# Kernel optimization log

Measured on AMD Instinct MI355X. Metric: run time of the kernel, lower is better.

Reference implementation:

```python
import jax, jax.numpy as jnp
import numpy as np

H = 16       # num_heads (groups for complex conv)
A = 32       # num frequency anchors
KSZ = 5      # complex conv kernel size
PAD = (KSZ - 1) // 2  # circular padding, matches ComplexConv1DLayer


def setup_inputs() -> dict:
    key = jax.random.key(0)
    ks = jax.random.split(key, 12)
    B, N, D = 4, 2048, 1024
    hid, ghid = 256, 256  # pooling MLP hidden, gate MLP hidden
    F = N // 2 + 1

    def rn(k, shp, s=0.02):
        return jax.random.normal(k, shp, jnp.float32) * s

    return {
        "x": jax.random.normal(ks[0], (B, N, D), jnp.float32),
        "Wv": rn(ks[1], (D, D)), "bv": jnp.zeros((D,), jnp.float32),
        "Wp1": rn(ks[2], (D, hid)), "bp1": jnp.zeros((hid,), jnp.float32),
        "Wp2": rn(ks[3], (hid, 1)), "bp2": jnp.zeros((1,), jnp.float32),
        "Wg1": rn(ks[4], (D, ghid)), "bg1": jnp.zeros((ghid,), jnp.float32),
        "Wg2": rn(ks[5], (ghid, 2 * H * A)), "bg2": jnp.zeros((2 * H * A,), jnp.float32),
        "mod_bias": jnp.zeros((F,), jnp.float32),
        "conv_kr": rn(ks[6], (KSZ,), 1.0 / np.sqrt(KSZ)),
        "conv_ki": rn(ks[7], (KSZ,), 1.0 / np.sqrt(KSZ)),
        "Wo": rn(ks[8], (D, D)), "bo": jnp.zeros((D,), jnp.float32),
    }


def reference(x, Wv, bv, Wp1, bp1, Wp2, bp2, Wg1, bg1, Wg2, bg2,
              mod_bias, conv_kr, conv_ki, Wo, bo):
    B, N, D = x.shape
    dh = D // H
    F = N // 2 + 1

    # value projection -> per-head sequences, rFFT over sequence axis
    v = (x @ Wv + bv).reshape(B, N, H, dh).transpose(0, 2, 1, 3)   # (B,H,N,dh)
    Vf = jnp.fft.rfft(v, axis=2)                                   # (B,H,F,dh) complex64

    # AttentionPoolingLayer: two-layer MLP scores -> softmax over seq -> weighted sum
    s = jax.nn.gelu(x @ Wp1 + bp1, approximate=False) @ Wp2 + bp2  # (B,N,1)
    w = jax.nn.softmax(s, axis=1)
    g = jnp.sum(x * w, axis=1)                                     # (B,D)

    # gate MLP -> complex anchors (B,H,A)
    a = (jax.nn.gelu(g @ Wg1 + bg1, approximate=False) @ Wg2 + bg2).reshape(B, H, A, 2)
    anch_r, anch_i = a[..., 0], a[..., 1]

    # ComplexInterpolationLayer: cubic interpolation of anchors to F bins
    gr = jax.image.resize(anch_r, (B, H, F), method="cubic")
    gi = jax.image.resize(anch_i, (B, H, F), method="cubic")
    gate = gr + 1j * gi                                            # (B,H,F)

    # ComplexModReLULayer: ReLU(|z|+b) * z / |z| with per-frequency bias
    mag = jnp.abs(gate)
    gate = gate * (jax.nn.relu(mag + mod_bias) / (mag + 1e-8))

    # ComplexConv1DLayer: circular-pad complex conv along frequency
    gp = jnp.concatenate([gate[..., -PAD:], gate, gate[..., :PAD]], axis=-1)
    ker = conv_kr.astype(jnp.complex64) + 1j * conv_ki.astype(jnp.complex64)
    gate = sum(ker[j] * gp[..., j:j + F] for j in range(KSZ))      # (B,H,F)

    # spectral gating + inverse FFT + output projection
    y = jnp.fft.irfft(Vf * gate[..., None], n=N, axis=2)           # (B,H,N,dh)
    y = y.transpose(0, 2, 1, 3).reshape(B, N, D)
    return y @ Wo + bo
```

## Files before the change

kernel.cpp:

```cpp
#include <hip/hip_runtime.h>
#include <math.h>

#define NSEQ 2048
#define DMOD 1024
#define NBATCH 4
#define NHEAD 16
#define NFREQ 1025

typedef unsigned short u16t;
typedef __attribute__((ext_vector_type(8))) short short8;
typedef __attribute__((ext_vector_type(4))) float f32x4;

__device__ __forceinline__ float gelu_exact(float x) {
  return 0.5f * x * (1.0f + erff(x * 0.70710678118654752440f));
}
__device__ __forceinline__ u16t bf16_rtn(float x) {
  unsigned u = __float_as_uint(x);
  return (u16t)((u + 0x7FFFu + ((u >> 16) & 1u)) >> 16);
}
__device__ __forceinline__ float bf16f(u16t h) {
  return __uint_as_float(((unsigned)h) << 16);
}
__device__ __forceinline__ void gload_lds16(const u16t* g, u16t* l) {
  __builtin_amdgcn_global_load_lds(
      (const __attribute__((address_space(1))) void*)g,
      (__attribute__((address_space(3))) void*)l, 16, 0, 0);
}

__global__ __launch_bounds__(256) void split_kernel(const float* __restrict__ in,
    u16t* __restrict__ hi, u16t* __restrict__ lo, int n8) {
  for (int i = blockIdx.x * blockDim.x + threadIdx.x; i < n8; i += gridDim.x * blockDim.x) {
    const float4* p = reinterpret_cast<const float4*>(in + (size_t)i * 8);
    float4 a = p[0], b = p[1];
    float vv[8] = {a.x, a.y, a.z, a.w, b.x, b.y, b.z, b.w};
    alignas(16) u16t th[8];
    alignas(16) u16t tl[8];
#pragma unroll
    for (int e = 0; e < 8; ++e) {
      u16t h = bf16_rtn(vv[e]);
      th[e] = h;
      tl[e] = bf16_rtn(vv[e] - bf16f(h));
    }
    *reinterpret_cast<uint4*>(hi + (size_t)i * 8) = *reinterpret_cast<const uint4*>(th);
    *reinterpret_cast<uint4*>(lo + (size_t)i * 8) = *reinterpret_cast<const uint4*>(tl);
  }
}

__global__ __launch_bounds__(256) void tsplit_kernel(const float* __restrict__ W,
    u16t* __restrict__ Th, u16t* __restrict__ Tl, int K, int N) {
  __shared__ float tile[32][33];
  int k0 = blockIdx.y * 32, n0 = blockIdx.x * 32;
  int r = threadIdx.x >> 5, c = threadIdx.x & 31;
#pragma unroll
  for (int i = 0; i < 4; ++i)
    tile[r + 8 * i][c] = W[(size_t)(k0 + r + 8 * i) * N + n0 + c];
  __syncthreads();
#pragma unroll
  for (int i = 0; i < 4; ++i) {
    int rr = r + 8 * i;
    float v = tile[c][rr];
    u16t h = bf16_rtn(v);
    Th[(size_t)(n0 + rr) * K + k0 + c] = h;
    Tl[(size_t)(n0 + rr) * K + k0 + c] = bf16_rtn(v - bf16f(h));
  }
}

__global__ __launch_bounds__(256) void gemm_fused_kernel(
    const u16t* __restrict__ Ah_g, const u16t* __restrict__ Al_g,
    const u16t* __restrict__ Bvh, const u16t* __restrict__ Bvl,
    const u16t* __restrict__ Bph, const u16t* __restrict__ Bpl,
    const float* __restrict__ bv, const float* __restrict__ bp1,
    const float* __restrict__ Wp2,
    float* __restrict__ vT, float* __restrict__ s_part) {
  __shared__ u16t Ahs[128 * 64], Als[128 * 64], Bhs[128 * 64], Bls[128 * 64];
  __shared__ u16t Php[32 * 64], Ppl[32 * 64];
  const int tid = threadIdx.x;
  const int lane = tid & 63, wave = tid >> 6;
  const int lr = lane & 15, lg = lane >> 4;
  const int wm0 = (wave >> 1) * 64, wn0 = (wave & 1) * 64;
  const int nwg = gridDim.x;
  const int L = (blockIdx.x & 7) * (nwg >> 3) + (blockIdx.x >> 3);
  const int m0 = (L >> 3) * 128;
  const int nblk = L & 7;
  const int n0 = nblk * 128;
  const int pc0 = nblk * 32;
  const int K = 1024;

  f32x4 acc[4][4];
#pragma unroll
  for (int i = 0; i < 4; ++i)
#pragma unroll
    for (int j = 0; j < 4; ++j) acc[i][j] = 0.0f;
  f32x4 accp[2][2];
#pragma unroll
  for (int i = 0; i < 2; ++i)
#pragma unroll
    for (int j = 0; j < 2; ++j) accp[i][j] = 0.0f;

  for (int k0 = 0; k0 < K; k0 += 64) {
#pragma unroll
    for (int q = 0; q < 4; ++q) {
      int cid = q * 256 + tid;
      int row = cid >> 3, grp = cid & 7;
      int koff = k0 + ((grp ^ (row & 7)) << 3);
      size_t ea = (size_t)(m0 + row) * K + koff;
      size_t eb = (size_t)(n0 + row) * K + koff;
      int lbase = q * 2048 + wave * 512;
      gload_lds16(Ah_g + ea, Ahs + lbase);
      gload_lds16(Al_g + ea, Als + lbase);
      gload_lds16(Bvh + eb, Bhs + lbase);
      gload_lds16(Bvl + eb, Bls + lbase);
    }
    {
      int row = tid >> 3, grp = tid & 7;
      int koff = k0 + ((grp ^ (row & 7)) << 3);
      size_t ep = (size_t)(pc0 + row) * K + koff;
      int lbase = wave * 512;
      gload_lds16(Bph + ep, Php + lbase);
      gload_lds16(Bpl + ep, Ppl + lbase);
    }
    __syncthreads();
#pragma unroll
    for (int kf = 0; kf < 2; ++kf) {
      short8 ah[4], al[4];
#pragma unroll
      for (int mi = 0; mi < 4; ++mi) {
        int r_ = wm0 + mi * 16 + lr;
        int g = (kf * 4 + lg) ^ (r_ & 7);
        ah[mi] = *reinterpret_cast<const short8*>(&Ahs[r_ * 64 + g * 8]);
        al[mi] = *reinterpret_cast<const short8*>(&Als[r_ * 64 + g * 8]);
      }
#pragma unroll
      for (int ni = 0; ni < 4; ++ni) {
        int r_ = wn0 + ni * 16 + lr;
        int g = (kf * 4 + lg) ^ (r_ & 7);
        short8 bh8 = *reinterpret_cast<const short8*>(&Bhs[r_ * 64 + g * 8]);
        short8 bl8 = *reinterpret_cast<const short8*>(&Bls[r_ * 64 + g * 8]);
#pragma unroll
        for (int mi = 0; mi < 4; ++mi) {
          acc[mi][ni] = __builtin_amdgcn_mfma_f32_16x16x32_bf16(ah[mi], bh8, acc[mi][ni], 0, 0, 0);
          acc[mi][ni] = __builtin_amdgcn_mfma_f32_16x16x32_bf16(ah[mi], bl8, acc[mi][ni], 0, 0, 0);
          acc[mi][ni] = __builtin_amdgcn_mfma_f32_16x16x32_bf16(al[mi], bh8, acc[mi][ni], 0, 0, 0);
        }
      }
      short8 pah[2], pal[2];
#pragma unroll
      for (int mi = 0; mi < 2; ++mi) {
        int r_ = wave * 32 + mi * 16 + lr;
        int g = (kf * 4 + lg) ^ (r_ & 7);
        pah[mi] = *reinterpret_cast<const short8*>(&Ahs[r_ * 64 + g * 8]);
        pal[mi] = *reinterpret_cast<const short8*>(&Als[r_ * 64 + g * 8]);
      }
#pragma unroll
      for (int ni = 0; ni < 2; ++ni) {
        int r_ = ni * 16 + lr;
        int g = (kf * 4 + lg) ^ (r_ & 7);
        short8 pbh = *reinterpret_cast<const short8*>(&Php[r_ * 64 + g * 8]);
        short8 pbl = *reinterpret_cast<const short8*>(&Ppl[r_ * 64 + g * 8]);
#pragma unroll
        for (int mi = 0; mi < 2; ++mi) {
          accp[mi][ni] = __builtin_amdgcn_mfma_f32_16x16x32_bf16(pah[mi], pbh, accp[mi][ni], 0, 0, 0);
          accp[mi][ni] = __builtin_amdgcn_mfma_f32_16x16x32_bf16(pah[mi], pbl, accp[mi][ni], 0, 0, 0);
          accp[mi][ni] = __builtin_amdgcn_mfma_f32_16x16x32_bf16(pal[mi], pbh, accp[mi][ni], 0, 0, 0);
        }
      }
    }
    __syncthreads();
  }
#pragma unroll
  for (int mi = 0; mi < 4; ++mi)
#pragma unroll
    for (int ni = 0; ni < 4; ++ni) {
      int col = n0 + wn0 + ni * 16 + lr;
      float bvv = bv[col];
      f32x4 a = acc[mi][ni];
      int mbase = m0 + wm0 + mi * 16 + lg * 4;
      int b = mbase >> 11, ss = mbase & 2047;
      float4 o4;
      o4.x = a[0] + bvv; o4.y = a[1] + bvv; o4.z = a[2] + bvv; o4.w = a[3] + bvv;
      *reinterpret_cast<float4*>(vT + (size_t)b * (DMOD * NSEQ) + (size_t)col * NSEQ + ss) = o4;
    }
  {
    float w2[2], bcol[2];
#pragma unroll
    for (int ni = 0; ni < 2; ++ni) {
      int col = pc0 + ni * 16 + lr;
      w2[ni] = Wp2[col];
      bcol[ni] = bp1[col];
    }
#pragma unroll
    for (int mi = 0; mi < 2; ++mi)
#pragma unroll
      for (int r = 0; r < 4; ++r) {
        float p = 0.f;
#pragma unroll
        for (int ni = 0; ni < 2; ++ni)
          p = fmaf(gelu_exact(accp[mi][ni][r] + bcol[ni]), w2[ni], p);
        p += __shfl_xor(p, 1);
        p += __shfl_xor(p, 2);
        p += __shfl_xor(p, 4);
        p += __shfl_xor(p, 8);
        if (lr == 0) {
          int row = m0 + wave * 32 + mi * 16 + lg * 4 + r;
          s_part[nblk * 8192 + row] = p;
        }
      }
  }
}

template<int NBLK>
__global__ __launch_bounds__(256) void mfma_gemm(
    const u16t* __restrict__ Ah_g, const u16t* __restrict__ Al_g,
    const u16t* __restrict__ Bh_g, const u16t* __restrict__ Bl_g,
    const float* __restrict__ bias,
    float* __restrict__ Cf,
    int N, int K) {
  __shared__ u16t Ahs[128 * 64], Als[128 * 64], Bhs[128 * 64], Bls[128 * 64];
  const int tid = threadIdx.x;
  const int lane = tid & 63, wave = tid >> 6;
  const int lr = lane & 15, lg = lane >> 4;
  const int wm0 = (wave >> 1) * 64, wn0 = (wave & 1) * 64;
  const int nwg = gridDim.x;
  const int L = (blockIdx.x & 7) * (nwg >> 3) + (blockIdx.x >> 3);
  const int m0 = (L / NBLK) * 128, n0 = (L % NBLK) * 128;

  f32x4 acc[4][4];
#pragma unroll
  for (int i = 0; i < 4; ++i)
#pragma unroll
    for (int j = 0; j < 4; ++j) acc[i][j] = 0.0f;

  for (int k0 = 0; k0 < K; k0 += 64) {
#pragma unroll
    for (int q = 0; q < 4; ++q) {
      int cid = q * 256 + tid;
      int row = cid >> 3, grp = cid & 7;
      int koff = k0 + ((grp ^ (row & 7)) << 3);
      size_t ea = (size_t)(m0 + row) * K + koff;
      size_t eb = (size_t)(n0 + row) * K + koff;
      int lbase = q * 2048 + wave * 512;
      gload_lds16(Ah_g + ea, Ahs + lbase);
      gload_lds16(Al_g + ea, Als + lbase);
      gload_lds16(Bh_g + eb, Bhs + lbase);
      gload_lds16(Bl_g + eb, Bls + lbase);
    }
    __syncthreads();
#pragma unroll
    for (int kf = 0; kf < 2; ++kf) {
      short8 ah[4], al[4];
#pragma unroll
      for (int mi = 0; mi < 4; ++mi) {
        int r_ = wm0 + mi * 16 + lr;
        int g = (kf * 4 + lg) ^ (r_ & 7);
        ah[mi] = *reinterpret_cast<const short8*>(&Ahs[r_ * 64 + g * 8]);
        al[mi] = *reinterpret_cast<const short8*>(&Als[r_ * 64 + g * 8]);
      }
#pragma unroll
      for (int ni = 0; ni < 4; ++ni) {
        int r_ = wn0 + ni * 16 + lr;
        int g = (kf * 4 + lg) ^ (r_ & 7);
        short8 bh8 = *reinterpret_cast<const short8*>(&Bhs[r_ * 64 + g * 8]);
        short8 bl8 = *reinterpret_cast<const short8*>(&Bls[r_ * 64 + g * 8]);
#pragma unroll
        for (int mi = 0; mi < 4; ++mi) {
          acc[mi][ni] = __builtin_amdgcn_mfma_f32_16x16x32_bf16(ah[mi], bh8, acc[mi][ni], 0, 0, 0);
          acc[mi][ni] = __builtin_amdgcn_mfma_f32_16x16x32_bf16(ah[mi], bl8, acc[mi][ni], 0, 0, 0);
          acc[mi][ni] = __builtin_amdgcn_mfma_f32_16x16x32_bf16(al[mi], bh8, acc[mi][ni], 0, 0, 0);
        }
      }
    }
    __syncthreads();
  }
#pragma unroll
  for (int mi = 0; mi < 4; ++mi)
#pragma unroll
    for (int ni = 0; ni < 4; ++ni) {
      int col = n0 + wn0 + ni * 16 + lr;
      float bvv = bias[col];
      f32x4 a = acc[mi][ni];
#pragma unroll
      for (int r = 0; r < 4; ++r) {
        int row = m0 + wm0 + mi * 16 + lg * 4 + r;
        Cf[(size_t)row * N + col] = a[r] + bvv;
      }
    }
}

#define PADI(i) ((i) + ((i) >> 5))

template<int HJ, int TWS>
__device__ __forceinline__ void fwd_reg_stage(float* vr, float* vi,
    const float* TWr, const float* TWi, int lane) {
  float twr_[HJ], twi_[HJ];
#pragma unroll
  for (int t = 0; t < HJ; ++t) {
    int m = (t * 64 + lane) * TWS;
    twr_[t] = TWr[PADI(m)]; twi_[t] = TWi[PADI(m)];
  }
#pragma unroll
  for (int j = 0; j < 16; ++j) {
    if (j & HJ) continue;
    int t = j & (HJ - 1);
    float ur = vr[j], ui = vi[j];
    float wr = vr[j + HJ], wi = vi[j + HJ];
    float dr = ur - wr, di = ui - wi;
    vr[j] = ur + wr; vi[j] = ui + wi;
    vr[j + HJ] = dr * twr_[t] - di * twi_[t];
    vi[j + HJ] = dr * twi_[t] + di * twr_[t];
  }
}

template<int S, int TWS>
__device__ __forceinline__ void fwd_lane_stage(float* vr, float* vi,
    const float* TWr, const float* TWi, int lane) {
  float twr_ = 1.0f, twi_ = 0.0f;
  if (S > 1) {
    int m = (lane & (S - 1)) * TWS;
    twr_ = TWr[PADI(m)]; twi_ = TWi[PADI(m)];
  }
  bool hi = (lane & S) != 0;
#pragma unroll
  for (int j = 0; j < 16; ++j) {
    float or_ = __shfl_xor(vr[j], S, 64);
    float oi_ = __shfl_xor(vi[j], S, 64);
    float sr = vr[j] + or_, si_ = vi[j] + oi_;
    float dr = or_ - vr[j], di = oi_ - vi[j];
    float rr = dr * twr_ - di * twi_;
    float ri = dr * twi_ + di * twr_;
    vr[j] = hi ? rr : sr;
    vi[j] = hi ? ri : si_;
  }
}

template<int S, int TWS>
__device__ __forceinline__ void inv_lane_stage(float* vr, float* vi,
    const float* TWr, const float* TWi, int lane) {
  float twr_ = 1.0f, twi_ = 0.0f;
  if (S > 1) {
    int m = (lane & (S - 1)) * TWS;
    twr_ = TWr[PADI(m)]; twi_ = -TWi[PADI(m)];
  }
  bool hi = (lane & S) != 0;
#pragma unroll
  for (int j = 0; j < 16; ++j) {
    float xr = vr[j], xi = vi[j];
    if (S > 1) {
      float pr = xr * twr_ - xi * twi_;
      float pi = xr * twi_ + xi * twr_;
      xr = hi ? pr : xr;
      xi = hi ? pi : xi;
    }
    float or_ = __shfl_xor(xr, S, 64);
    float oi_ = __shfl_xor(xi, S, 64);
    vr[j] = hi ? (or_ - xr) : (xr + or_);
    vi[j] = hi ? (oi_ - xi) : (xi + oi_);
  }
}

template<int HJ, int TWS>
__device__ __forceinline__ void inv_reg_stage(float* vr, float* vi,
    const float* TWr, const float* TWi, int lane) {
  float twr_[HJ], twi_[HJ];
#pragma unroll
  for (int t = 0; t < HJ; ++t) {
    int m = (t * 64 + lane) * TWS;
    twr_[t] = TWr[PADI(m)]; twi_[t] = -TWi[PADI(m)];
  }
#pragma unroll
  for (int j = 0; j < 16; ++j) {
    if (j & HJ) continue;
    int t = j & (HJ - 1);
    float ur = vr[j], ui = vi[j];
    float br = vr[j + HJ], bi = vi[j + HJ];
    float wr = br * twr_[t] - bi * twi_[t];
    float wi = br * twi_[t] + bi * twr_[t];
    vr[j] = ur + wr; vi[j] = ui + wi;
    vr[j + HJ] = ur - wr; vi[j + HJ] = ui - wi;
  }
}

__global__ __launch_bounds__(256) void conv_fft_kernel(
    float* __restrict__ vio, const float* __restrict__ gateb) {
  __shared__ float Zr[4][1056], Zi[4][1056];
  __shared__ float TWr[528], TWi[528];
  const int tid = threadIdx.x;
  const int lane = tid & 63, wave = tid >> 6;
  const int c0 = blockIdx.x * 4;
  const int b = blockIdx.y;
  const int bh = b * NHEAD + (c0 >> 6);
  const float* gate_bh = gateb + (size_t)bh * NFREQ * 2;

#pragma unroll
  for (int q = 0; q < 2; ++q) {
    int m = q * 256 + tid;
    float si, co;
    sincosf(-3.14159265358979323846f * (float)m * (1.0f / 512.0f), &si, &co);
    TWr[PADI(m)] = co; TWi[PADI(m)] = si;
  }
  __syncthreads();

  float* zr = Zr[wave];
  float* zi = Zi[wave];
  float* col = vio + ((size_t)b * DMOD + (c0 + wave)) * NSEQ;

  float vr[16], vi[16];
#pragma unroll
  for (int j = 0; j < 16; ++j) {
    float2 w2 = *reinterpret_cast<const float2*>(col + 2 * (j * 64 + lane));
    vr[j] = w2.x; vi[j] = w2.y;
  }

  fwd_reg_stage<8, 1>(vr, vi, TWr, TWi, lane);
  fwd_reg_stage<4, 2>(vr, vi, TWr, TWi, lane);
  fwd_reg_stage<2, 4>(vr, vi, TWr, TWi, lane);
  fwd_reg_stage<1, 8>(vr, vi, TWr, TWi, lane);
  fwd_lane_stage<32, 16>(vr, vi, TWr, TWi, lane);
  fwd_lane_stage<16, 32>(vr, vi, TWr, TWi, lane);
  fwd_lane_stage<8, 64>(vr, vi, TWr, TWi, lane);
  fwd_lane_stage<4, 128>(vr, vi, TWr, TWi, lane);
  fwd_lane_stage<2, 256>(vr, vi, TWr, TWi, lane);
  fwd_lane_stage<1, 0>(vr, vi, TWr, TWi, lane);

#pragma unroll
  for (int j = 0; j < 16; ++j) {
    int p = PADI(j * 64 + lane);
    zr[p] = vr[j]; zi[p] = vi[j];
  }
  asm volatile("s_waitcnt lgkmcnt(0)" ::: "memory");

  const float s1 = 1.0f / 1024.0f;
#pragma unroll
  for (int q = 0; q < 8; ++q) {
    int k = q * 64 + lane;
    if (k == 0) {
      float z0r = zr[0], z0i = zi[0];
      float X0 = z0r + z0i;
      float XN = z0r - z0i;
      float2 G0 = *reinterpret_cast<const float2*>(gate_bh + 0);
      float2 GN = *reinterpret_cast<const float2*>(gate_bh + 1024 * 2);
      float y0 = X0 * G0.x * s1;
      float yN = XN * GN.x * s1;
      zr[0] = 0.5f * (y0 + yN); zi[0] = 0.5f * (y0 - yN);
      float zmr = zr[1], zmi = zi[1];
      float X5r = zmr, X5i = -zmi;
      float2 G5 = *reinterpret_cast<const float2*>(gate_bh + 512 * 2);
      float Y5r = (X5r * G5.x - X5i * G5.y) * s1;
      float Y5i = (X5r * G5.y + X5i * G5.x) * s1;
      zr[1] = Y5r; zi[1] = -Y5i;
    } else {
      int kq = 1024 - k;
      int rp = PADI((int)(__brev((unsigned)k) >> 22));
      int rq = PADI((int)(__brev((unsigned)kq) >> 22));
      float Zkr = zr[rp], Zki = zi[rp];
      float Zqr = zr[rq], Zqi = zi[rq];
      float Er = 0.5f * (Zkr + Zqr), Ei = 0.5f * (Zki - Zqi);
      float Odr = 0.5f * (Zki + Zqi), Odi = -0.5f * (Zkr - Zqr);
      float ti, tr;
      sincosf(-3.14159265358979323846f * (float)k * (1.0f / 1024.0f), &ti, &tr);
      float Pr = Odr * tr - Odi * ti, Pi = Odr * ti + Odi * tr;
      float Xkr = Er + Pr, Xki = Ei + Pi;
      float Xqr = Er - Pr, Xqi = -(Ei - Pi);
      float2 Gk = *reinterpret_cast<const float2*>(gate_bh + k * 2);
      float2 Gq = *reinterpret_cast<const float2*>(gate_bh + kq * 2);
      float Ykr = (Xkr * Gk.x - Xki * Gk.y) * s1;
      float Yki = (Xkr * Gk.y + Xki * Gk.x) * s1;
      float Yqr = (Xqr * Gq.x - Xqi * Gq.y) * s1;
      float Yqi = (Xqr * Gq.y + Xqi * Gq.x) * s1;
      float E2r = 0.5f * (Ykr + Yqr), E2i = 0.5f * (Yki - Yqi);
      float D2r = 0.5f * (Ykr - Yqr), D2i = 0.5f * (Yki + Yqi);
      float O2r = D2r * tr + D2i * ti, O2i = D2i * tr - D2r * ti;
      zr[rp] = E2r - O2i; zi[rp] = E2i + O2r;
      zr[rq] = E2r + O2i; zi[rq] = O2r - E2i;
    }
  }
  asm volatile("s_waitcnt lgkmcnt(0)" ::: "memory");

#pragma unroll
  for (int j = 0; j < 16; ++j) {
    int p = PADI(j * 64 + lane);
    vr[j] = zr[p]; vi[j] = zi[p];
  }
  asm volatile("s_waitcnt lgkmcnt(0)" ::: "memory");

  inv_lane_stage<1, 0>(vr, vi, TWr, TWi, lane);
  inv_lane_stage<2, 256>(vr, vi, TWr, TWi, lane);
  inv_lane_stage<4, 128>(vr, vi, TWr, TWi, lane);
  inv_lane_stage<8, 64>(vr, vi, TWr, TWi, lane);
  inv_lane_stage<16, 32>(vr, vi, TWr, TWi, lane);
  inv_lane_stage<32, 16>(vr, vi, TWr, TWi, lane);
  inv_reg_stage<1, 8>(vr, vi, TWr, TWi, lane);
  inv_reg_stage<2, 4>(vr, vi, TWr, TWi, lane);
  inv_reg_stage<4, 2>(vr, vi, TWr, TWi, lane);
  inv_reg_stage<8, 1>(vr, vi, TWr, TWi, lane);

#pragma unroll
  for (int j = 0; j < 16; ++j) {
    *reinterpret_cast<float2*>(col + 2 * (j * 64 + lane)) = make_float2(vr[j], vi[j]);
  }
}

__global__ __launch_bounds__(256) void tysplit_kernel(
    const float* __restrict__ yT, u16t* __restrict__ yh, u16t* __restrict__ yl) {
  __shared__ float tile[64][65];
  int t0 = blockIdx.x * 64, c0 = blockIdx.y * 64, b = blockIdx.z;
  int r = threadIdx.x >> 4;
  int cc = (threadIdx.x & 15) * 4;
#pragma unroll
  for (int i = 0; i < 4; ++i) {
    int row = r + 16 * i;
    float4 w = *reinterpret_cast<const float4*>(
        yT + ((size_t)b * DMOD + c0 + row) * NSEQ + t0 + cc);
    tile[row][cc] = w.x; tile[row][cc + 1] = w.y;
    tile[row][cc + 2] = w.z; tile[row][cc + 3] = w.w;
  }
  __syncthreads();
#pragma unroll
  for (int i = 0; i < 4; ++i) {
    int tt = r + 16 * i;
    alignas(8) u16t hh[4], ll[4];
#pragma unroll
    for (int e = 0; e < 4; ++e) {
      float v = tile[cc + e][tt];
      u16t h = bf16_rtn(v);
      hh[e] = h;
      ll[e] = bf16_rtn(v - bf16f(h));
    }
    size_t o = ((size_t)b * NSEQ + t0 + tt) * DMOD + c0 + cc;
    *reinterpret_cast<ushort4*>(yh + o) = *reinterpret_cast<const ushort4*>(hh);
    *reinterpret_cast<ushort4*>(yl + o) = *reinterpret_cast<const ushort4*>(ll);
  }
}

__global__ __launch_bounds__(256) void softmax_stats_kernel(
    const float* __restrict__ s_part, const float* __restrict__ bp2,
    float* __restrict__ s, float* __restrict__ bstats) {
  int b = blockIdx.x, tid = threadIdx.x;
  __shared__ float red[256];
  float bp = bp2[0];
  float m = -1e30f;
  for (int n = tid; n < NSEQ; n += 256) {
    int row = b * NSEQ + n;
    float v = bp;
#pragma unroll
    for (int c = 0; c < 8; ++c) v += s_part[c * 8192 + row];
    s[row] = v;
    m = fmaxf(m, v);
  }
  red[tid] = m; __syncthreads();
  for (int o = 128; o; o >>= 1) { if (tid < o) red[tid] = fmaxf(red[tid], red[tid + o]); __syncthreads(); }
  float bm = red[0]; __syncthreads();
  float sum = 0.f;
  for (int n = tid; n < NSEQ; n += 256) sum += expf(s[b * NSEQ + n] - bm);
  red[tid] = sum; __syncthreads();
  for (int o = 128; o; o >>= 1) { if (tid < o) red[tid] += red[tid + o]; __syncthreads(); }
  if (tid == 0) { bstats[b * 2] = bm; bstats[b * 2 + 1] = red[0]; }
}

__global__ __launch_bounds__(256) void pool_partial_kernel(
    const float* __restrict__ x, const float* __restrict__ s,
    const float* __restrict__ bstats, float* __restrict__ gpart) {
  int chunk = blockIdx.x, b = blockIdx.y;
  int tid = threadIdx.x;
  __shared__ float wsh[128];
  float bm = bstats[b * 2], inv = 1.0f / bstats[b * 2 + 1];
  int n0 = chunk * 128;
  if (tid < 128) wsh[tid] = expf(s[b * NSEQ + n0 + tid] - bm) * inv;
  __syncthreads();
  float acc[4] = {};
  for (int n = 0; n < 128; ++n) {
    float wn = wsh[n];
    const float* xr = &x[((size_t)b * NSEQ + n0 + n) * DMOD];
#pragma unroll
    for (int q = 0; q < 4; ++q) acc[q] = fmaf(wn, xr[tid + 256 * q], acc[q]);
  }
  float* gp = &gpart[((size_t)b * 16 + chunk) * DMOD];
#pragma unroll
  for (int q = 0; q < 4; ++q) gp[tid + 256 * q] = acc[q];
}

__global__ __launch_bounds__(256) void pool_reduce_mlp1_kernel(
    const float* __restrict__ gpart, const float* __restrict__ Wg1,
    float* __restrict__ part1) {
  int kb = blockIdx.x, b = blockIdx.y;
  int tid = threadIdx.x;
  int k0 = kb * 64;
  __shared__ float g_s[64];
  if (tid < 64) {
    float acc = 0.f;
#pragma unroll
    for (int j = 0; j < 16; ++j)
      acc += gpart[((size_t)b * 16 + j) * DMOD + k0 + tid];
    g_s[tid] = acc;
  }
  __syncthreads();
  float acc = 0.f;
#pragma unroll 8
  for (int i = 0; i < 64; ++i)
    acc = fmaf(g_s[i], Wg1[(size_t)(k0 + i) * 256 + tid], acc);
  part1[((size_t)b * 16 + kb) * 256 + tid] = acc;
}

__global__ __launch_bounds__(256) void mlp1red_mlp2_kernel(
    const float* __restrict__ part1, const float* __restrict__ bg1,
    const float* __restrict__ Wg2, float* __restrict__ part2) {
  int kb2 = blockIdx.x, nh = blockIdx.y, b = blockIdx.z;
  int tid = threadIdx.x;
  int k0 = kb2 * 64;
  __shared__ float hs_s[64];
  if (tid < 64) {
    float acc = bg1[k0 + tid];
#pragma unroll
    for (int j = 0; j < 16; ++j)
      acc += part1[((size_t)b * 16 + j) * 256 + k0 + tid];
    hs_s[tid] = gelu_exact(acc);
  }
  __syncthreads();
  float acc[2] = {};
#pragma unroll 8
  for (int i = 0; i < 64; ++i) {
    float hv = hs_s[i];
    const float* wr = &Wg2[(size_t)(k0 + i) * 1024 + nh * 512];
    acc[0] = fmaf(hv, wr[tid], acc[0]);
    acc[1] = fmaf(hv, wr[tid + 256], acc[1]);
  }
  float* pp = &part2[((size_t)b * 4 + kb2) * 1024 + nh * 512];
  pp[tid] = acc[0];
  pp[tid + 256] = acc[1];
}

__device__ __forceinline__ float keys_cubic(float x) {
  if (x >= 2.0f) return 0.0f;
  if (x >= 1.0f) return ((-0.5f * x + 2.5f) * x - 4.0f) * x + 2.0f;
  return ((1.5f * x - 2.5f) * x) * x + 1.0f;
}

__global__ __launch_bounds__(256) void gate_kernel(
    const float* __restrict__ part2, const float* __restrict__ bg2,
    const float* __restrict__ mod_bias,
    const float* __restrict__ kr5, const float* __restrict__ ki5,
    float* __restrict__ gate_out) {
  int bh = blockIdx.x;
  int tid = threadIdx.x;
  __shared__ float anch_s[64];
  __shared__ float ar_[32], ai_[32];
  __shared__ float gr[NFREQ], gi[NFREQ];
  int b = bh >> 4, h = bh & 15;
  if (tid < 64) {
    int cc = h * 64 + tid;
    float acc = bg2[cc];
#pragma unroll
    for (int j = 0; j < 4; ++j)
      acc += part2[((size_t)b * 4 + j) * 1024 + cc];
    anch_s[tid] = acc;
  }
  __syncthreads();
  if (tid < 32) {
    ar_[tid] = anch_s[tid * 2 + 0];
    ai_[tid] = anch_s[tid * 2 + 1];
  }
  __syncthreads();
  const float inv_scale = 32.0f / 1025.0f;
  for (int f = tid; f < NFREQ; f += 256) {
    float c = (f + 0.5f) * inv_scale - 0.5f;
    int j0 = (int)floorf(c) - 1;
    float wr = 0.f, wi = 0.f, wsum = 0.f;
#pragma unroll
    for (int u = 0; u < 4; ++u) {
      int j = j0 + u;
      if (j < 0 || j > 31) continue;
      float w = keys_cubic(fabsf(c - (float)j));
      wsum += w;
      wr = fmaf(w, ar_[j], wr);
      wi = fmaf(w, ai_[j], wi);
    }
    float invw = 1.0f / wsum;
    wr *= invw; wi *= invw;
    float mag = sqrtf(wr * wr + wi * wi);
    float scale = fmaxf(mag + mod_bias[f], 0.0f) / (mag + 1e-8f);
    gr[f] = wr * scale;
    gi[f] = wi * scale;
  }
  __syncthreads();
  float k_r[5], k_i[5];
#pragma unroll
  for (int j = 0; j < 5; ++j) { k_r[j] = kr5[j]; k_i[j] = ki5[j]; }
  for (int f = tid; f < NFREQ; f += 256) {
    float cr = 0.f, ci = 0.f;
#pragma unroll
    for (int j = 0; j < 5; ++j) {
      int idx = f + j - 2;
      if (idx < 0) idx += NFREQ;
      else if (idx >= NFREQ) idx -= NFREQ;
      float a = gr[idx], bb = gi[idx];
      cr = fmaf(k_r[j], a, cr); cr = fmaf(-k_i[j], bb, cr);
      ci = fmaf(k_r[j], bb, ci); ci = fmaf(k_i[j], a, ci);
    }
    gate_out[((size_t)bh * NFREQ + f) * 2 + 0] = cr;
    gate_out[((size_t)bh * NFREQ + f) * 2 + 1] = ci;
  }
}

extern "C" void kernel_launch(void* const* d_in, const int* in_sizes, int n_in,
                              void* d_out, int out_size, void* d_ws, size_t ws_size,
                              hipStream_t stream) {
  const float* x        = (const float*)d_in[0];
  const float* Wv       = (const float*)d_in[1];
  const float* bv       = (const float*)d_in[2];
  const float* Wp1      = (const float*)d_in[3];
  const float* bp1      = (const float*)d_in[4];
  const float* Wp2      = (const float*)d_in[5];
  const float* bp2      = (const float*)d_in[6];
  const float* Wg1      = (const float*)d_in[7];
  const float* bg1      = (const float*)d_in[8];
  const float* Wg2      = (const float*)d_in[9];
  const float* bg2      = (const float*)d_in[10];
  const float* mod_bias = (const float*)d_in[11];
  const float* ckr      = (const float*)d_in[12];
  const float* cki      = (const float*)d_in[13];
  const float* Wo       = (const float*)d_in[14];
  const float* bo       = (const float*)d_in[15];

  const int M = NBATCH * NSEQ;
  const size_t MD = (size_t)M * DMOD;
  char* wsb = (char*)d_ws;

  u16t* x_hi = (u16t*)wsb;
  u16t* x_lo = x_hi + MD;
  u16t* y_hi = x_hi;
  u16t* y_lo = x_lo;
  u16t* WT_h = (u16t*)(wsb + (size_t)32 * 1024 * 1024);
  u16t* WT_l = (u16t*)(wsb + (size_t)34 * 1024 * 1024);
  u16t* WTp1_h = (u16t*)(wsb + (size_t)36 * 1024 * 1024);
  u16t* WTp1_l = (u16t*)(wsb + (size_t)36 * 1024 * 1024 + 524288);
  float* s_part = (float*)(wsb + (size_t)37 * 1024 * 1024);
  float* s      = (float*)(wsb + (size_t)36 * 1024 * 1024);
  float* bstats = s + 8192;
  float* gpart  = bstats + 16;
  float* part1 = (float*)(wsb + (size_t)32 * 1024 * 1024);
  float* part2 = part1 + 4 * 16 * 256;
  float* gateb = (float*)(wsb + (size_t)32 * 1024 * 1024 + 65536);

  float* vT  = (float*)d_out;
  float* out = (float*)d_out;

  dim3 blk(256);

  split_kernel<<<dim3(2048), blk, 0, stream>>>(x, x_hi, x_lo, (int)(MD / 8));
  tsplit_kernel<<<dim3(1024 / 32, 1024 / 32), blk, 0, stream>>>(Wv, WT_h, WT_l, 1024, 1024);
  tsplit_kernel<<<dim3(256 / 32, 1024 / 32), blk, 0, stream>>>(Wp1, WTp1_h, WTp1_l, 1024, 256);
  gemm_fused_kernel<<<dim3(512), blk, 0, stream>>>(
      x_hi, x_lo, WT_h, WT_l, WTp1_h, WTp1_l, bv, bp1, Wp2, vT, s_part);
  softmax_stats_kernel<<<dim3(NBATCH), blk, 0, stream>>>(s_part, bp2, s, bstats);
  pool_partial_kernel<<<dim3(16, NBATCH), blk, 0, stream>>>(x, s, bstats, gpart);
  pool_reduce_mlp1_kernel<<<dim3(16, NBATCH), blk, 0, stream>>>(gpart, Wg1, part1);
  mlp1red_mlp2_kernel<<<dim3(4, 2, NBATCH), blk, 0, stream>>>(part1, bg1, Wg2, part2);
  gate_kernel<<<dim3(NBATCH * NHEAD), blk, 0, stream>>>(part2, bg2, mod_bias, ckr, cki, gateb);
  conv_fft_kernel<<<dim3(DMOD / 4, NBATCH), blk, 0, stream>>>(vT, gateb);
  tysplit_kernel<<<dim3(NSEQ / 64, DMOD / 64, NBATCH), blk, 0, stream>>>(vT, y_hi, y_lo);
  tsplit_kernel<<<dim3(1024 / 32, 1024 / 32), blk, 0, stream>>>(Wo, WT_h, WT_l, 1024, 1024);
  mfma_gemm<8><<<dim3((DMOD / 128) * (M / 128)), blk, 0, stream>>>(
      y_hi, y_lo, WT_h, WT_l, bo, out, DMOD, 1024);
}
```

Before: 206.0 us.

## Fuse small pooling/gate kernels and merge weight-split launches to cut launch count

Merges the Wv and Wp1 transpose-split launches into one kernel and folds the softmax statistics into each pool_partial block, which now recomputes the per-batch max and sum redundantly. It also moves the second gate MLP layer into gate_kernel and drops the separate mlp1red_mlp2 launch. The Wo split is moved earlier, into the slot after the fused GEMM, and workspace pointers are re-laid out so its buffers do not collide. The aim is fewer tiny serialized launches, at the cost of redundant softmax work in every block and a serial 256-term dot product per thread in gate_kernel.

```diff
diff --git a/kernel.cpp b/kernel.cpp
--- a/kernel.cpp
+++ b/kernel.cpp
@@ -50,6 +50,31 @@
     u16t* __restrict__ Th, u16t* __restrict__ Tl, int K, int N) {
   __shared__ float tile[32][33];
   int k0 = blockIdx.y * 32, n0 = blockIdx.x * 32;
+  int r = threadIdx.x >> 5, c = threadIdx.x & 31;
+#pragma unroll
+  for (int i = 0; i < 4; ++i)
+    tile[r + 8 * i][c] = W[(size_t)(k0 + r + 8 * i) * N + n0 + c];
+  __syncthreads();
+#pragma unroll
+  for (int i = 0; i < 4; ++i) {
+    int rr = r + 8 * i;
+    float v = tile[c][rr];
+    u16t h = bf16_rtn(v);
+    Th[(size_t)(n0 + rr) * K + k0 + c] = h;
+    Tl[(size_t)(n0 + rr) * K + k0 + c] = bf16_rtn(v - bf16f(h));
+  }
+}
+
+__global__ __launch_bounds__(256) void tsplit2_kernel(
+    const float* __restrict__ Wv, u16t* __restrict__ Tvh, u16t* __restrict__ Tvl,
+    const float* __restrict__ Wp, u16t* __restrict__ Tph, u16t* __restrict__ Tpl) {
+  __shared__ float tile[32][33];
+  int bx = blockIdx.x;
+  const float* W; u16t* Th; u16t* Tl; int N, n0;
+  if (bx < 32) { W = Wv; Th = Tvh; Tl = Tvl; N = 1024; n0 = bx * 32; }
+  else         { W = Wp; Th = Tph; Tl = Tpl; N = 256;  n0 = (bx - 32) * 32; }
+  const int K = 1024;
+  int k0 = blockIdx.y * 32;
   int r = threadIdx.x >> 5, c = threadIdx.x & 31;
 #pragma unroll
   for (int i = 0; i < 4; ++i)
@@ -531,40 +556,43 @@
   }
 }
 
-__global__ __launch_bounds__(256) void softmax_stats_kernel(
-    const float* __restrict__ s_part, const float* __restrict__ bp2,
-    float* __restrict__ s, float* __restrict__ bstats) {
-  int b = blockIdx.x, tid = threadIdx.x;
+__global__ __launch_bounds__(256) void pool_partial_kernel(
+    const float* __restrict__ x, const float* __restrict__ s_part,
+    const float* __restrict__ bp2, float* __restrict__ gpart) {
+  int chunk = blockIdx.x, b = blockIdx.y;
+  int tid = threadIdx.x;
   __shared__ float red[256];
+  __shared__ float wsh[128];
   float bp = bp2[0];
+  float sv[8];
   float m = -1e30f;
-  for (int n = tid; n < NSEQ; n += 256) {
-    int row = b * NSEQ + n;
+#pragma unroll
+  for (int q = 0; q < 8; ++q) {
+    int row = b * NSEQ + q * 256 + tid;
     float v = bp;
 #pragma unroll
     for (int c = 0; c < 8; ++c) v += s_part[c * 8192 + row];
-    s[row] = v;
+    sv[q] = v;
     m = fmaxf(m, v);
   }
   red[tid] = m; __syncthreads();
   for (int o = 128; o; o >>= 1) { if (tid < o) red[tid] = fmaxf(red[tid], red[tid + o]); __syncthreads(); }
   float bm = red[0]; __syncthreads();
   float sum = 0.f;
-  for (int n = tid; n < NSEQ; n += 256) sum += expf(s[b * NSEQ + n] - bm);
+#pragma unroll
+  for (int q = 0; q < 8; ++q) sum += expf(sv[q] - bm);
   red[tid] = sum; __syncthreads();
   for (int o = 128; o; o >>= 1) { if (tid < o) red[tid] += red[tid + o]; __syncthreads(); }
-  if (tid == 0) { bstats[b * 2] = bm; bstats[b * 2 + 1] = red[0]; }
-}
-
-__global__ __launch_bounds__(256) void pool_partial_kernel(
-    const float* __restrict__ x, const float* __restrict__ s,
-    const float* __restrict__ bstats, float* __restrict__ gpart) {
-  int chunk = blockIdx.x, b = blockIdx.y;
-  int tid = threadIdx.x;
-  __shared__ float wsh[128];
-  float bm = bstats[b * 2], inv = 1.0f / bstats[b * 2 + 1];
+  float inv = 1.0f / red[0];
+  __syncthreads();
   int n0 = chunk * 128;
-  if (tid < 128) wsh[tid] = expf(s[b * NSEQ + n0 + tid] - bm) * inv;
+  if (tid < 128) {
+    int row = b * NSEQ + n0 + tid;
+    float v = bp;
+#pragma unroll
+    for (int c = 0; c < 8; ++c) v += s_part[c * 8192 + row];
+    wsh[tid] = expf(v - bm) * inv;
+  }
   __syncthreads();
   float acc[4] = {};
   for (int n = 0; n < 128; ++n) {
@@ -600,34 +628,6 @@
   part1[((size_t)b * 16 + kb) * 256 + tid] = acc;
 }
 
-__global__ __launch_bounds__(256) void mlp1red_mlp2_kernel(
-    const float* __restrict__ part1, const float* __restrict__ bg1,
-    const float* __restrict__ Wg2, float* __restrict__ part2) {
-  int kb2 = blockIdx.x, nh = blockIdx.y, b = blockIdx.z;
-  int tid = threadIdx.x;
-  int k0 = kb2 * 64;
-  __shared__ float hs_s[64];
-  if (tid < 64) {
-    float acc = bg1[k0 + tid];
-#pragma unroll
-    for (int j = 0; j < 16; ++j)
-      acc += part1[((size_t)b * 16 + j) * 256 + k0 + tid];
-    hs_s[tid] = gelu_exact(acc);
-  }
-  __syncthreads();
-  float acc[2] = {};
-#pragma unroll 8
-  for (int i = 0; i < 64; ++i) {
-    float hv = hs_s[i];
-    const float* wr = &Wg2[(size_t)(k0 + i) * 1024 + nh * 512];
-    acc[0] = fmaf(hv, wr[tid], acc[0]);
-    acc[1] = fmaf(hv, wr[tid + 256], acc[1]);
-  }
-  float* pp = &part2[((size_t)b * 4 + kb2) * 1024 + nh * 512];
-  pp[tid] = acc[0];
-  pp[tid + 256] = acc[1];
-}
-
 __device__ __forceinline__ float keys_cubic(float x) {
   if (x >= 2.0f) return 0.0f;
   if (x >= 1.0f) return ((-0.5f * x + 2.5f) * x - 4.0f) * x + 2.0f;
@@ -635,23 +635,31 @@
 }
 
 __global__ __launch_bounds__(256) void gate_kernel(
-    const float* __restrict__ part2, const float* __restrict__ bg2,
+    const float* __restrict__ part1, const float* __restrict__ bg1,
+    const float* __restrict__ Wg2, const float* __restrict__ bg2,
     const float* __restrict__ mod_bias,
     const float* __restrict__ kr5, const float* __restrict__ ki5,
     float* __restrict__ gate_out) {
   int bh = blockIdx.x;
   int tid = threadIdx.x;
+  __shared__ float hs_s[256];
   __shared__ float anch_s[64];
   __shared__ float ar_[32], ai_[32];
   __shared__ float gr[NFREQ], gi[NFREQ];
   int b = bh >> 4, h = bh & 15;
+  {
+    float a1 = bg1[tid];
+#pragma unroll
+    for (int j = 0; j < 16; ++j)
+      a1 += part1[((size_t)b * 16 + j) * 256 + tid];
+    hs_s[tid] = gelu_exact(a1);
+  }
+  __syncthreads();
   if (tid < 64) {
     int cc = h * 64 + tid;
-    float acc = bg2[cc];
-#pragma unroll
-    for (int j = 0; j < 4; ++j)
-      acc += part2[((size_t)b * 4 + j) * 1024 + cc];
-    anch_s[tid] = acc;
+    float a2 = bg2[cc];
+    for (int i = 0; i < 256; ++i) a2 = fmaf(hs_s[i], Wg2[(size_t)i * 1024 + cc], a2);
+    anch_s[tid] = a2;
   }
   __syncthreads();
   if (tid < 32) {
@@ -733,12 +741,9 @@
   u16t* WTp1_h = (u16t*)(wsb + (size_t)36 * 1024 * 1024);
   u16t* WTp1_l = (u16t*)(wsb + (size_t)36 * 1024 * 1024 + 524288);
   float* s_part = (float*)(wsb + (size_t)37 * 1024 * 1024);
-  float* s      = (float*)(wsb + (size_t)36 * 1024 * 1024);
-  float* bstats = s + 8192;
-  float* gpart  = bstats + 16;
-  float* part1 = (float*)(wsb + (size_t)32 * 1024 * 1024);
-  float* part2 = part1 + 4 * 16 * 256;
-  float* gateb = (float*)(wsb + (size_t)32 * 1024 * 1024 + 65536);
+  float* gpart = (float*)(wsb + (size_t)36 * 1024 * 1024);
+  float* part1 = gpart + 65536;
+  float* gateb = part1 + 4096;
 
   float* vT  = (float*)d_out;
   float* out = (float*)d_out;
@@ -746,18 +751,16 @@
   dim3 blk(256);
 
   split_kernel<<<dim3(2048), blk, 0, stream>>>(x, x_hi, x_lo, (int)(MD / 8));
-  tsplit_kernel<<<dim3(1024 / 32, 1024 / 32), blk, 0, stream>>>(Wv, WT_h, WT_l, 1024, 1024);
-  tsplit_kernel<<<dim3(256 / 32, 1024 / 32), blk, 0, stream>>>(Wp1, WTp1_h, WTp1_l, 1024, 256);
+  tsplit2_kernel<<<dim3(40, 32), blk, 0, stream>>>(Wv, WT_h, WT_l, Wp1, WTp1_h, WTp1_l);
   gemm_fused_kernel<<<dim3(512), blk, 0, stream>>>(
       x_hi, x_lo, WT_h, WT_l, WTp1_h, WTp1_l, bv, bp1, Wp2, vT, s_part);
-  softmax_stats_kernel<<<dim3(NBATCH), blk, 0, stream>>>(s_part, bp2, s, bstats);
-  pool_partial_kernel<<<dim3(16, NBATCH), blk, 0, stream>>>(x, s, bstats, gpart);
+  tsplit_kernel<<<dim3(1024 / 32, 1024 / 32), blk, 0, stream>>>(Wo, WT_h, WT_l, 1024, 1024);
+  pool_partial_kernel<<<dim3(16, NBATCH), blk, 0, stream>>>(x, s_part, bp2, gpart);
   pool_reduce_mlp1_kernel<<<dim3(16, NBATCH), blk, 0, stream>>>(gpart, Wg1, part1);
-  mlp1red_mlp2_kernel<<<dim3(4, 2, NBATCH), blk, 0, stream>>>(part1, bg1, Wg2, part2);
-  gate_kernel<<<dim3(NBATCH * NHEAD), blk, 0, stream>>>(part2, bg2, mod_bias, ckr, cki, gateb);
+  gate_kernel<<<dim3(NBATCH * NHEAD), blk, 0, stream>>>(
+      part1, bg1, Wg2, bg2, mod_bias, ckr, cki, gateb);
   conv_fft_kernel<<<dim3(DMOD / 4, NBATCH), blk, 0, stream>>>(vT, gateb);
   tysplit_kernel<<<dim3(NSEQ / 64, DMOD / 64, NBATCH), blk, 0, stream>>>(vT, y_hi, y_lo);
-  tsplit_kernel<<<dim3(1024 / 32, 1024 / 32), blk, 0, stream>>>(Wo, WT_h, WT_l, 1024, 1024);
   mfma_gemm<8><<<dim3((DMOD / 128) * (M / 128)), blk, 0, stream>>>(
       y_hi, y_lo, WT_h, WT_l, bo, out, DMOD, 1024);
 }
```

Result: no change. 204.0 us (-1.0%).
